# Kernel optimization log

Hardware: AMD Instinct MI355X
Metric: run time of the kernel (lower is better)

## Reference

```python
import jax, jax.numpy as jnp
import numpy as np

B = 16384
RNN = 256       # rnn_hidden_dim
LAT = 64        # action_latent_dim
ATT = 64        # attention_dim
A = 32          # n_actions
HID = 256       # nn_hidden_size
LEAKY_SLOPE = 0.01  # nn.LeakyReLU default


def _linear_init(key, out_f, in_f):
    # torch nn.Linear default init: U(-1/sqrt(in_f), 1/sqrt(in_f))
    kw, kb = jax.random.split(key)
    bound = 1.0 / np.sqrt(in_f)
    w = jax.random.uniform(kw, (out_f, in_f), jnp.float32, -bound, bound)
    b = jax.random.uniform(kb, (out_f,), jnp.float32, -bound, bound)
    return w, b


def setup_inputs() -> dict:
    key = jax.random.key(0)
    ks = jax.random.split(key, 8)
    h = jax.random.normal(ks[0], (B, RNN), jnp.float32)
    action_latent = jax.random.normal(ks[1], (A, LAT), jnp.float32)
    q_fc_w, q_fc_b = _linear_init(ks[2], LAT, RNN)
    msg_w1, msg_b1 = _linear_init(ks[3], HID, RNN + LAT)
    msg_w2, msg_b2 = _linear_init(ks[4], A, HID)
    key_w, key_b = _linear_init(ks[5], ATT, RNN)
    query_w, query_b = _linear_init(ks[6], ATT, LAT)
    return {
        "h": h, "action_latent": action_latent,
        "q_fc_w": q_fc_w, "q_fc_b": q_fc_b,
        "msg_w1": msg_w1, "msg_b1": msg_b1,
        "msg_w2": msg_w2, "msg_b2": msg_b2,
        "key_w": key_w, "key_b": key_b,
        "query_w": query_w, "query_b": query_b,
    }


def reference(h, action_latent, q_fc_w, q_fc_b, msg_w1, msg_b1,
              msg_w2, msg_b2, key_w, key_b, query_w, query_b):
    # role_key = q_fc(h): [B, LAT];  q[b,a] = action_latent[a] . role_key[b]
    role_key = h @ q_fc_w.T + q_fc_b
    q = jnp.einsum('al,bl->ba', action_latent, role_key)  # [B, A]

    # msg_net(cat([h_repeat, action_latent], -1)): split the first Linear over
    # the concat halves to avoid materializing the [B, A, RNN+LAT] buffer.
    w1_h, w1_a = msg_w1[:, :RNN], msg_w1[:, RNN:]
    pre = (h @ w1_h.T)[:, None, :] + (action_latent @ w1_a.T)[None, :, :] + msg_b1
    hid = jnp.where(pre >= 0, pre, LEAKY_SLOPE * pre)      # [B, A, HID]
    msg = hid @ msg_w2.T + msg_b2                          # [B, A, A]

    # Attention: key row is identical across the expanded n_actions dim, so
    # alpha[b,i,:] == softmax_j(key[b].query[j]) for every i. gated_msg.sum(1)
    # therefore equals sm[b,:] * msg.sum(dim=1).
    key = h @ key_w.T + key_b                              # [B, ATT]
    query = action_latent @ query_w.T + query_b            # [A, ATT]
    scores = (key / jnp.sqrt(jnp.float32(ATT))) @ query.T  # [B, A]
    sm = jax.nn.softmax(scores, axis=-1)

    return q + sm * msg.sum(axis=1)                        # [B, A]
```

## Files before the change

### kernel.cpp

```cpp
#include <hip/hip_runtime.h>
#include <math.h>

#define BB    16384
#define RNN   256
#define LAT   64
#define ATTD  64
#define NA    32
#define HID   256
#define NCOL  384
#define TBR   16
#define KP    264
#define RKP   72
#define SLOPE 0.01f

#define WS_VT 50688
#define WS_W2 58880
#define WS_AL 62976
#define WS_QY 64000

typedef __attribute__((ext_vector_type(8))) short bf16x8;
typedef __attribute__((ext_vector_type(4))) float f32x4;
typedef __attribute__((ext_vector_type(8))) unsigned short ushort8;

__device__ __forceinline__ unsigned short f2bf(float x) {
    union { float f; unsigned u; } c; c.f = x;
    unsigned r = c.u + 0x7FFFu + ((c.u >> 16) & 1u);
    return (unsigned short)(r >> 16);
}

__global__ __launch_bounds__(256) void prep_kernel(
    const float* __restrict__ AL,
    const float* __restrict__ q_fc_w,
    const float* __restrict__ msg_w1,
    const float* __restrict__ msg_b1,
    const float* __restrict__ msg_w2,
    const float* __restrict__ key_w,
    const float* __restrict__ query_w,
    const float* __restrict__ query_b,
    float* __restrict__ ws)
{
    const int tid = blockIdx.x * 256 + threadIdx.x;
    const int nth = gridDim.x * 256;
    unsigned short* Wb  = (unsigned short*)ws;
    float*          VT  = ws + WS_VT;
    unsigned short* W2b = (unsigned short*)(ws + WS_W2);
    unsigned short* ALb = (unsigned short*)(ws + WS_AL);
    unsigned short* Qyb = (unsigned short*)(ws + WS_QY);

    for (int idx = tid; idx < NCOL * 256; idx += nth) {
        const int j = idx >> 8, k = idx & 255;
        float v;
        if (j < 256)      v = msg_w1[j * 320 + k];
        else if (j < 320) v = q_fc_w[(j - 256) * 256 + k];
        else              v = key_w[(j - 320) * 256 + k];
        Wb[j * KP + k] = f2bf(v);
    }
    for (int idx = tid; idx < HID * NA; idx += nth) {
        const int hc = idx >> 5, a = idx & 31;
        float s = msg_b1[hc];
        #pragma unroll 16
        for (int l = 0; l < LAT; ++l)
            s += AL[a * LAT + l] * msg_w1[hc * 320 + 256 + l];
        VT[idx] = s;
    }
    for (int idx = tid; idx < NA * HID; idx += nth)
        W2b[idx] = f2bf(msg_w2[idx]);
    for (int idx = tid; idx < NA * LAT; idx += nth)
        ALb[idx] = f2bf(AL[idx]);
    for (int idx = tid; idx < NA * ATTD; idx += nth) {
        const int a = idx >> 6, j = idx & 63;
        float s = query_b[j];
        #pragma unroll 16
        for (int l = 0; l < LAT; ++l)
            s += AL[a * LAT + l] * query_w[j * LAT + l];
        Qyb[idx] = f2bf(0.125f * s);
    }
}

__global__ __launch_bounds__(256, 4) void main_kernel(
    const float* __restrict__ h,
    const float* __restrict__ q_fc_b,
    const float* __restrict__ msg_b2,
    const float* __restrict__ key_b,
    const float* __restrict__ ws,
    float* __restrict__ out)
{
    __shared__ unsigned short hbuf[TBR * KP];
    __shared__ unsigned short Sb[TBR * KP];
    __shared__ unsigned short rkb[TBR * RKP];
    __shared__ unsigned short keyb[TBR * RKP];
    __shared__ float Scl[TBR * 33];
    __shared__ float ql[TBR * 33];
    __shared__ float stat_mx[TBR], stat_rd[TBR];

    const int t  = threadIdx.x;
    const int b0 = blockIdx.x * TBR;
    const short* Wbs = (const short*)ws;
    const float* VTf = ws + WS_VT;
    const short* W2s = (const short*)(ws + WS_W2);
    const short* ALs = (const short*)(ws + WS_AL);
    const short* Qys = (const short*)(ws + WS_QY);

    for (int g = t; g < TBR * 32; g += 256) {
        const int row = g >> 5, kc = (g & 31) << 3;
        const float4* p = (const float4*)(h + (size_t)(b0 + row) * RNN + kc);
        const float4 v0 = p[0], v1 = p[1];
        ushort8 u;
        u[0] = f2bf(v0.x); u[1] = f2bf(v0.y); u[2] = f2bf(v0.z); u[3] = f2bf(v0.w);
        u[4] = f2bf(v1.x); u[5] = f2bf(v1.y); u[6] = f2bf(v1.z); u[7] = f2bf(v1.w);
        *(ushort8*)(hbuf + row * KP + kc) = u;
    }
    __syncthreads();

    const int lane = t & 63, w = t >> 6;
    const int ln = lane & 15, quad = lane >> 4;

    f32x4 acc[6];
    #pragma unroll
    for (int nt = 0; nt < 6; ++nt) acc[nt] = (f32x4){0.f, 0.f, 0.f, 0.f};
    const short* hb = (const short*)hbuf;
    #pragma unroll
    for (int kk = 0; kk < 8; ++kk) {
        const int ko = kk * 32 + quad * 8;
        const bf16x8 af = *(const bf16x8*)(hb + ln * KP + ko);
        #pragma unroll
        for (int nt = 0; nt < 6; ++nt) {
            const int col = (w * 6 + nt) * 16 + ln;
            const bf16x8 bfr = *(const bf16x8*)(Wbs + col * KP + ko);
            acc[nt] = __builtin_amdgcn_mfma_f32_16x16x32_bf16(af, bfr, acc[nt], 0, 0, 0);
        }
    }

    #pragma unroll
    for (int nt = 0; nt < 6; ++nt) {
        const int colbase = (w * 6 + nt) * 16;
        const int col = colbase + ln;
        if (colbase < 256) {
            float vt[32];
            const float4* vp = (const float4*)(VTf + col * NA);
            #pragma unroll
            for (int i = 0; i < 8; ++i) {
                const float4 v = vp[i];
                vt[4*i] = v.x; vt[4*i+1] = v.y; vt[4*i+2] = v.z; vt[4*i+3] = v.w;
            }
            #pragma unroll
            for (int r = 0; r < 4; ++r) {
                const float u = acc[nt][r];
                float s = 0.f;
                #pragma unroll
                for (int a = 0; a < 32; ++a) {
                    const float pre = u + vt[a];
                    s += fmaxf(pre, SLOPE * pre);
                }
                Sb[(quad * 4 + r) * KP + col] = f2bf(s);
            }
        } else if (colbase < 320) {
            const int k = col - 256;
            const float bias = q_fc_b[k];
            #pragma unroll
            for (int r = 0; r < 4; ++r)
                rkb[(quad * 4 + r) * RKP + k] = f2bf(acc[nt][r] + bias);
        } else {
            const int k = col - 320;
            const float bias = key_b[k];
            #pragma unroll
            for (int r = 0; r < 4; ++r)
                keyb[(quad * 4 + r) * RKP + k] = f2bf(acc[nt][r] + bias);
        }
    }
    __syncthreads();

    f32x4 mc = (f32x4){0.f, 0.f, 0.f, 0.f};
    if (w < 2) {
        const short* Sbs = (const short*)Sb;
        #pragma unroll
        for (int kk = 0; kk < 8; ++kk) {
            const int ko = kk * 32 + quad * 8;
            const bf16x8 af = *(const bf16x8*)(Sbs + ln * KP + ko);
            const bf16x8 bfr = *(const bf16x8*)(W2s + (w * 16 + ln) * HID + ko);
            mc = __builtin_amdgcn_mfma_f32_16x16x32_bf16(af, bfr, mc, 0, 0, 0);
        }
    } else {
        const int na = w - 2;
        f32x4 qc = (f32x4){0.f, 0.f, 0.f, 0.f};
        f32x4 sc = (f32x4){0.f, 0.f, 0.f, 0.f};
        const short* rks = (const short*)rkb;
        const short* kys = (const short*)keyb;
        #pragma unroll
        for (int kk = 0; kk < 2; ++kk) {
            const int ko = kk * 32 + quad * 8;
            const bf16x8 aq = *(const bf16x8*)(rks + ln * RKP + ko);
            const bf16x8 bq = *(const bf16x8*)(ALs + (na * 16 + ln) * LAT + ko);
            qc = __builtin_amdgcn_mfma_f32_16x16x32_bf16(aq, bq, qc, 0, 0, 0);
            const bf16x8 ak = *(const bf16x8*)(kys + ln * RKP + ko);
            const bf16x8 bk = *(const bf16x8*)(Qys + (na * 16 + ln) * LAT + ko);
            sc = __builtin_amdgcn_mfma_f32_16x16x32_bf16(ak, bk, sc, 0, 0, 0);
        }
        const int a = na * 16 + ln;
        #pragma unroll
        for (int r = 0; r < 4; ++r) {
            ql [(quad * 4 + r) * 33 + a] = qc[r];
            Scl[(quad * 4 + r) * 33 + a] = sc[r];
        }
    }
    __syncthreads();

    if (t < TBR) {
        const float* srow = Scl + t * 33;
        float mx = -1e30f;
        #pragma unroll
        for (int i = 0; i < NA; ++i) mx = fmaxf(mx, srow[i]);
        float den = 0.f;
        #pragma unroll
        for (int i = 0; i < NA; ++i) den += __expf(srow[i] - mx);
        stat_mx[t] = mx;
        stat_rd[t] = 1.f / den;
    }
    __syncthreads();

    if (w < 2) {
        const int a = w * 16 + ln;
        const float b2 = 32.f * msg_b2[a];
        #pragma unroll
        for (int r = 0; r < 4; ++r) {
            const int row = quad * 4 + r;
            const float sm = __expf(Scl[row * 33 + a] - stat_mx[row]) * stat_rd[row];
            out[(size_t)(b0 + row) * NA + a] = ql[row * 33 + a] + sm * (mc[r] + b2);
        }
    }
}

extern "C" void kernel_launch(void* const* d_in, const int* in_sizes, int n_in,
                              void* d_out, int out_size, void* d_ws, size_t ws_size,
                              hipStream_t stream) {
    const float* h        = (const float*)d_in[0];
    const float* AL       = (const float*)d_in[1];
    const float* q_fc_w   = (const float*)d_in[2];
    const float* q_fc_b   = (const float*)d_in[3];
    const float* msg_w1   = (const float*)d_in[4];
    const float* msg_b1   = (const float*)d_in[5];
    const float* msg_w2   = (const float*)d_in[6];
    const float* msg_b2   = (const float*)d_in[7];
    const float* key_w    = (const float*)d_in[8];
    const float* key_b    = (const float*)d_in[9];
    const float* query_w  = (const float*)d_in[10];
    const float* query_b  = (const float*)d_in[11];
    float* out = (float*)d_out;
    float* ws  = (float*)d_ws;

    prep_kernel<<<128, 256, 0, stream>>>(AL, q_fc_w, msg_w1, msg_b1, msg_w2,
                                         key_w, query_w, query_b, ws);
    main_kernel<<<BB / TBR, 256, 0, stream>>>(h, q_fc_b, msg_b2, key_b, ws, out);
}
```

Before: 125.0 us.

## Rewrite LeakyReLU sum via abs identity and pre-pack weights in MFMA fragment layout

The per-element LeakyReLU reduction over 32 actions is rewritten with the exact identity leaky(x) = 0.505x + 0.495|x|. The linear part collapses to a precomputed per-column sum (SV), so the inner loop only accumulates absolute values, cutting VALU work per element. Weight matrices (W1/q_fc/key, W2, action latents, query) are pre-packed in the prep kernel into lane-contiguous MFMA fragment order, so B-fragment loads are coalesced. The h A-fragments are held in registers and the GEMM is restructured per column group. The result can differ slightly from before because of different rounding order, and the kernel uses more registers.

```diff
diff --git a/kernel.cpp b/kernel.cpp
--- a/kernel.cpp
+++ b/kernel.cpp
@@ -7,16 +7,15 @@
 #define ATTD  64
 #define NA    32
 #define HID   256
-#define NCOL  384
 #define TBR   16
 #define KP    264
 #define RKP   72
-#define SLOPE 0.01f
-
-#define WS_VT 50688
-#define WS_W2 58880
-#define WS_AL 62976
-#define WS_QY 64000
+
+#define WS_VT  49152
+#define WS_SV  57344
+#define WS_W2P 57600
+#define WS_ALP 61696
+#define WS_QYP 62720
 
 typedef __attribute__((ext_vector_type(8))) short bf16x8;
 typedef __attribute__((ext_vector_type(4))) float f32x4;
@@ -41,19 +40,30 @@
 {
     const int tid = blockIdx.x * 256 + threadIdx.x;
     const int nth = gridDim.x * 256;
-    unsigned short* Wb  = (unsigned short*)ws;
+    unsigned short* Wp  = (unsigned short*)ws;
     float*          VT  = ws + WS_VT;
-    unsigned short* W2b = (unsigned short*)(ws + WS_W2);
-    unsigned short* ALb = (unsigned short*)(ws + WS_AL);
-    unsigned short* Qyb = (unsigned short*)(ws + WS_QY);
-
-    for (int idx = tid; idx < NCOL * 256; idx += nth) {
-        const int j = idx >> 8, k = idx & 255;
-        float v;
-        if (j < 256)      v = msg_w1[j * 320 + k];
-        else if (j < 320) v = q_fc_w[(j - 256) * 256 + k];
-        else              v = key_w[(j - 320) * 256 + k];
-        Wb[j * KP + k] = f2bf(v);
+    float*          SV  = ws + WS_SV;
+    unsigned short* W2p = (unsigned short*)(ws + WS_W2P);
+    unsigned short* ALp = (unsigned short*)(ws + WS_ALP);
+    unsigned short* Qyp = (unsigned short*)(ws + WS_QYP);
+
+    for (int pos = tid; pos < 24 * 8 * 64; pos += nth) {
+        const int lane = pos & 63, kkg = pos >> 6;
+        const int kk = kkg & 7, g = kkg >> 3;
+        const int ln = lane & 15, quad = lane >> 4;
+        const int col = g * 16 + ln;
+        const int k0  = kk * 32 + quad * 8;
+        ushort8 u;
+        #pragma unroll
+        for (int j = 0; j < 8; ++j) {
+            const int k = k0 + j;
+            float v;
+            if (col < 256)      v = msg_w1[col * 320 + k];
+            else if (col < 320) v = q_fc_w[(col - 256) * 256 + k];
+            else                v = key_w[(col - 320) * 256 + k];
+            u[j] = f2bf(v);
+        }
+        *(ushort8*)(Wp + pos * 8) = u;
     }
     for (int idx = tid; idx < HID * NA; idx += nth) {
         const int hc = idx >> 5, a = idx & 31;
@@ -63,17 +73,52 @@
             s += AL[a * LAT + l] * msg_w1[hc * 320 + 256 + l];
         VT[idx] = s;
     }
-    for (int idx = tid; idx < NA * HID; idx += nth)
-        W2b[idx] = f2bf(msg_w2[idx]);
-    for (int idx = tid; idx < NA * LAT; idx += nth)
-        ALb[idx] = f2bf(AL[idx]);
-    for (int idx = tid; idx < NA * ATTD; idx += nth) {
-        const int a = idx >> 6, j = idx & 63;
-        float s = query_b[j];
-        #pragma unroll 16
-        for (int l = 0; l < LAT; ++l)
-            s += AL[a * LAT + l] * query_w[j * LAT + l];
-        Qyb[idx] = f2bf(0.125f * s);
+    for (int hc = tid; hc < HID; hc += nth) {
+        float s = 32.f * msg_b1[hc];
+        for (int l = 0; l < LAT; ++l) {
+            float asum = 0.f;
+            #pragma unroll
+            for (int a = 0; a < NA; ++a) asum += AL[a * LAT + l];
+            s += asum * msg_w1[hc * 320 + 256 + l];
+        }
+        SV[hc] = s;
+    }
+    for (int pos = tid; pos < 2 * 8 * 64; pos += nth) {
+        const int lane = pos & 63, kkh = pos >> 6;
+        const int kk = kkh & 7, half = kkh >> 3;
+        const int ln = lane & 15, quad = lane >> 4;
+        const int a = half * 16 + ln, k0 = kk * 32 + quad * 8;
+        ushort8 u;
+        #pragma unroll
+        for (int j = 0; j < 8; ++j) u[j] = f2bf(msg_w2[a * HID + k0 + j]);
+        *(ushort8*)(W2p + pos * 8) = u;
+    }
+    for (int pos = tid; pos < 2 * 2 * 64; pos += nth) {
+        const int lane = pos & 63, kkh = pos >> 6;
+        const int kk = kkh & 1, half = kkh >> 1;
+        const int ln = lane & 15, quad = lane >> 4;
+        const int a = half * 16 + ln, k0 = kk * 32 + quad * 8;
+        ushort8 u;
+        #pragma unroll
+        for (int j = 0; j < 8; ++j) u[j] = f2bf(AL[a * LAT + k0 + j]);
+        *(ushort8*)(ALp + pos * 8) = u;
+    }
+    for (int pos = tid; pos < 2 * 2 * 64; pos += nth) {
+        const int lane = pos & 63, kkh = pos >> 6;
+        const int kk = kkh & 1, half = kkh >> 1;
+        const int ln = lane & 15, quad = lane >> 4;
+        const int a = half * 16 + ln, k0 = kk * 32 + quad * 8;
+        ushort8 u;
+        #pragma unroll
+        for (int j = 0; j < 8; ++j) {
+            const int jj = k0 + j;
+            float s = query_b[jj];
+            #pragma unroll 16
+            for (int l = 0; l < LAT; ++l)
+                s += AL[a * LAT + l] * query_w[jj * LAT + l];
+            u[j] = f2bf(0.125f * s);
+        }
+        *(ushort8*)(Qyp + pos * 8) = u;
     }
 }
 
@@ -95,13 +140,16 @@
 
     const int t  = threadIdx.x;
     const int b0 = blockIdx.x * TBR;
-    const short* Wbs = (const short*)ws;
-    const float* VTf = ws + WS_VT;
-    const short* W2s = (const short*)(ws + WS_W2);
-    const short* ALs = (const short*)(ws + WS_AL);
-    const short* Qys = (const short*)(ws + WS_QY);
-
-    for (int g = t; g < TBR * 32; g += 256) {
+    const short* Wps  = (const short*)ws;
+    const float* VTf  = ws + WS_VT;
+    const float* SVf  = ws + WS_SV;
+    const short* W2ps = (const short*)(ws + WS_W2P);
+    const short* ALps = (const short*)(ws + WS_ALP);
+    const short* Qyps = (const short*)(ws + WS_QYP);
+
+    #pragma unroll
+    for (int i = 0; i < 2; ++i) {
+        const int g = t + i * 256;
         const int row = g >> 5, kc = (g & 31) << 3;
         const float4* p = (const float4*)(h + (size_t)(b0 + row) * RNN + kc);
         const float4 v0 = p[0], v1 = p[1];
@@ -115,57 +163,62 @@
     const int lane = t & 63, w = t >> 6;
     const int ln = lane & 15, quad = lane >> 4;
 
-    f32x4 acc[6];
+    const short* hb = (const short*)hbuf;
+    bf16x8 af[8];
     #pragma unroll
-    for (int nt = 0; nt < 6; ++nt) acc[nt] = (f32x4){0.f, 0.f, 0.f, 0.f};
-    const short* hb = (const short*)hbuf;
+    for (int kk = 0; kk < 8; ++kk)
+        af[kk] = *(const bf16x8*)(hb + ln * KP + kk * 32 + quad * 8);
+
     #pragma unroll
-    for (int kk = 0; kk < 8; ++kk) {
-        const int ko = kk * 32 + quad * 8;
-        const bf16x8 af = *(const bf16x8*)(hb + ln * KP + ko);
-        #pragma unroll
-        for (int nt = 0; nt < 6; ++nt) {
-            const int col = (w * 6 + nt) * 16 + ln;
-            const bf16x8 bfr = *(const bf16x8*)(Wbs + col * KP + ko);
-            acc[nt] = __builtin_amdgcn_mfma_f32_16x16x32_bf16(af, bfr, acc[nt], 0, 0, 0);
-        }
-    }
-
-    #pragma unroll
-    for (int nt = 0; nt < 6; ++nt) {
-        const int colbase = (w * 6 + nt) * 16;
-        const int col = colbase + ln;
-        if (colbase < 256) {
-            float vt[32];
+    for (int gi = 0; gi < 6; ++gi) {
+        const int g   = w + gi * 4;
+        const int col = g * 16 + ln;
+        const short* bp = Wps + (size_t)g * 4096 + lane * 8;
+
+        float vt[32];
+        float c1 = 0.f;
+        if (gi < 4) {
             const float4* vp = (const float4*)(VTf + col * NA);
             #pragma unroll
             for (int i = 0; i < 8; ++i) {
                 const float4 v = vp[i];
                 vt[4*i] = v.x; vt[4*i+1] = v.y; vt[4*i+2] = v.z; vt[4*i+3] = v.w;
             }
+            c1 = 0.505f * SVf[col];
+        }
+
+        f32x4 acc = (f32x4){0.f, 0.f, 0.f, 0.f};
+        #pragma unroll
+        for (int kk = 0; kk < 8; ++kk) {
+            const bf16x8 bfr = *(const bf16x8*)(bp + kk * 512);
+            acc = __builtin_amdgcn_mfma_f32_16x16x32_bf16(af[kk], bfr, acc, 0, 0, 0);
+        }
+
+        if (gi < 4) {
             #pragma unroll
             for (int r = 0; r < 4; ++r) {
-                const float u = acc[nt][r];
-                float s = 0.f;
+                const float u = acc[r];
+                float s0 = 0.f, s1 = 0.f;
                 #pragma unroll
-                for (int a = 0; a < 32; ++a) {
-                    const float pre = u + vt[a];
-                    s += fmaxf(pre, SLOPE * pre);
+                for (int a = 0; a < 32; a += 2) {
+                    s0 += __builtin_fabsf(u + vt[a]);
+                    s1 += __builtin_fabsf(u + vt[a + 1]);
                 }
-                Sb[(quad * 4 + r) * KP + col] = f2bf(s);
+                const float S = fmaf(16.16f, u, c1) + 0.495f * (s0 + s1);
+                Sb[(quad * 4 + r) * KP + col] = f2bf(S);
             }
-        } else if (colbase < 320) {
+        } else if (gi == 4) {
             const int k = col - 256;
             const float bias = q_fc_b[k];
             #pragma unroll
             for (int r = 0; r < 4; ++r)
-                rkb[(quad * 4 + r) * RKP + k] = f2bf(acc[nt][r] + bias);
+                rkb[(quad * 4 + r) * RKP + k] = f2bf(acc[r] + bias);
         } else {
             const int k = col - 320;
             const float bias = key_b[k];
             #pragma unroll
             for (int r = 0; r < 4; ++r)
-                keyb[(quad * 4 + r) * RKP + k] = f2bf(acc[nt][r] + bias);
+                keyb[(quad * 4 + r) * RKP + k] = f2bf(acc[r] + bias);
         }
     }
     __syncthreads();
@@ -175,32 +228,39 @@
         const short* Sbs = (const short*)Sb;
         #pragma unroll
         for (int kk = 0; kk < 8; ++kk) {
-            const int ko = kk * 32 + quad * 8;
-            const bf16x8 af = *(const bf16x8*)(Sbs + ln * KP + ko);
-            const bf16x8 bfr = *(const bf16x8*)(W2s + (w * 16 + ln) * HID + ko);
-            mc = __builtin_amdgcn_mfma_f32_16x16x32_bf16(af, bfr, mc, 0, 0, 0);
+            const bf16x8 afr = *(const bf16x8*)(Sbs + ln * KP + kk * 32 + quad * 8);
+            const bf16x8 bfr = *(const bf16x8*)(W2ps + ((w * 8 + kk) * 64 + lane) * 8);
+            mc = __builtin_amdgcn_mfma_f32_16x16x32_bf16(afr, bfr, mc, 0, 0, 0);
+        }
+    } else if (w == 2) {
+        const short* rks = (const short*)rkb;
+        #pragma unroll
+        for (int half = 0; half < 2; ++half) {
+            f32x4 qc = (f32x4){0.f, 0.f, 0.f, 0.f};
+            #pragma unroll
+            for (int kk = 0; kk < 2; ++kk) {
+                const bf16x8 aq = *(const bf16x8*)(rks + ln * RKP + kk * 32 + quad * 8);
+                const bf16x8 bq = *(const bf16x8*)(ALps + ((half * 2 + kk) * 64 + lane) * 8);
+                qc = __builtin_amdgcn_mfma_f32_16x16x32_bf16(aq, bq, qc, 0, 0, 0);
+            }
+            #pragma unroll
+            for (int r = 0; r < 4; ++r)
+                ql[(quad * 4 + r) * 33 + half * 16 + ln] = qc[r];
         }
     } else {
-        const int na = w - 2;
-        f32x4 qc = (f32x4){0.f, 0.f, 0.f, 0.f};
-        f32x4 sc = (f32x4){0.f, 0.f, 0.f, 0.f};
-        const short* rks = (const short*)rkb;
         const short* kys = (const short*)keyb;
         #pragma unroll
-        for (int kk = 0; kk < 2; ++kk) {
-            const int ko = kk * 32 + quad * 8;
-            const bf16x8 aq = *(const bf16x8*)(rks + ln * RKP + ko);
-            const bf16x8 bq = *(const bf16x8*)(ALs + (na * 16 + ln) * LAT + ko);
-            qc = __builtin_amdgcn_mfma_f32_16x16x32_bf16(aq, bq, qc, 0, 0, 0);
-            const bf16x8 ak = *(const bf16x8*)(kys + ln * RKP + ko);
-            const bf16x8 bk = *(const bf16x8*)(Qys + (na * 16 + ln) * LAT + ko);
-            sc = __builtin_amdgcn_mfma_f32_16x16x32_bf16(ak, bk, sc, 0, 0, 0);
-        }
-        const int a = na * 16 + ln;
-        #pragma unroll
-        for (int r = 0; r < 4; ++r) {
-            ql [(quad * 4 + r) * 33 + a] = qc[r];
-            Scl[(quad * 4 + r) * 33 + a] = sc[r];
+        for (int half = 0; half < 2; ++half) {
+            f32x4 sc = (f32x4){0.f, 0.f, 0.f, 0.f};
+            #pragma unroll
+            for (int kk = 0; kk < 2; ++kk) {
+                const bf16x8 ak = *(const bf16x8*)(kys + ln * RKP + kk * 32 + quad * 8);
+                const bf16x8 bk = *(const bf16x8*)(Qyps + ((half * 2 + kk) * 64 + lane) * 8);
+                sc = __builtin_amdgcn_mfma_f32_16x16x32_bf16(ak, bk, sc, 0, 0, 0);
+            }
+            #pragma unroll
+            for (int r = 0; r < 4; ++r)
+                Scl[(quad * 4 + r) * 33 + half * 16 + ln] = sc[r];
         }
     }
     __syncthreads();
```

Result: slower. 146.5 us (+17.2%).
